# Kernel optimization log

Hardware: AMD Instinct MI355X
Metric: run time of the kernel (lower is better)

The kernel has to match this reference:

```python
import jax, jax.numpy as jnp
import numpy as np

B, T = 4, 1024
H, C, DK, DV = 12, 4096, 64, 64
DIM = H * DK  # 768


def setup_inputs() -> dict:
    key = jax.random.key(0)
    k1, k2, k3 = jax.random.split(key, 3)
    x = jax.random.normal(k1, (B, T, DIM), dtype=jnp.float32)
    # key_embed initialized with kaiming_uniform in torch; uniform in [-bound, bound]
    bound = float(np.sqrt(3.0) * np.sqrt(2.0) / np.sqrt(C * DK))
    key_embed = jax.random.uniform(k2, (H, C, DK), minval=-bound, maxval=bound, dtype=jnp.float32)
    values = jax.random.normal(k3, (H, C, DV), dtype=jnp.float32)
    mask = jnp.ones((B, T), dtype=jnp.int32)
    return {"x": x, "mask": mask, "key_embed": key_embed, "values": values, "key_optim": 0}


def reference(x, mask, key_embed, values, key_optim):
    # x: [b, t, h*dk]; key_embed: [h, c, dk]; values: [h, c, dv]
    b, t, _ = x.shape
    h, c, dk = key_embed.shape
    dv = values.shape[-1]
    x = x.astype(jnp.float32)
    # 'b t (h d) -> h (b t) d'
    xh = x.reshape(b, t, h, dk).transpose(2, 0, 1, 3).reshape(h, b * t, dk)
    # squared-L2 nearest codebook entry (argmax of -cdist == argmin of squared dist)
    x2 = jnp.sum(xh * xh, axis=-1, keepdims=True)          # [h, n, 1]
    e2 = jnp.sum(key_embed * key_embed, axis=-1)           # [h, c]
    dots = jnp.einsum('hnd,hcd->hnc', xh, key_embed)       # [h, n, c]
    d2 = x2 - 2.0 * dots + e2[:, None, :]                  # [h, n, c]
    ind = jnp.argmin(d2, axis=-1)                          # [h, n]
    # gather per-head learned values: values[h, ind[h, n], :]
    memories = jnp.take_along_axis(values, ind[..., None], axis=1)  # [h, n, dv]
    # 'h (b t) dv -> b t (h dv)'  (decoder == 'mlp')
    memories = memories.transpose(1, 0, 2).reshape(b, t, h * dv)
    return memories
```

## Files before the change

### kernel.cpp

```cpp
#include <hip/hip_runtime.h>


#define HEADS 12
#define CODES 4096
#define DKI   64
#define DVI   64
#define DIMX  768
#define TAUS  3.84e-3f
#define WLCAP 32768
#define NPARTS 16

typedef _Float16 f16x8 __attribute__((ext_vector_type(8)));
typedef float f32x4 __attribute__((ext_vector_type(4)));

__device__ __forceinline__ unsigned short f2bf(float f) {
    unsigned int u = __float_as_uint(f);
    return (unsigned short)((u + 0x7fff + ((u >> 16) & 1)) >> 16);
}
__device__ __forceinline__ unsigned short f2h(float f) {
    _Float16 h = (_Float16)f;
    unsigned short u;
    __builtin_memcpy(&u, &h, 2);
    return u;
}
__device__ __forceinline__ f16x8 as_f16x8(uint4 v) {
    union { uint4 u; f16x8 h; } c; c.u = v; return c.h;
}

__device__ __forceinline__ float np_sumsq64(const float* __restrict__ a) {
#pragma clang fp contract(off)
    float r[8];
#pragma unroll
    for (int j = 0; j < 8; ++j) r[j] = a[j] * a[j];
#pragma unroll
    for (int i = 8; i < 64; i += 8)
#pragma unroll
        for (int j = 0; j < 8; ++j) r[j] += a[i + j] * a[i + j];
    return ((r[0] + r[1]) + (r[2] + r[3])) + ((r[4] + r[5]) + (r[6] + r[7]));
}

__device__ __forceinline__ float np_dot64(const float* __restrict__ xx,
                                          const float* __restrict__ ee) {
#pragma clang fp contract(off)
    float S0 = 0.f, S1 = 0.f, S2 = 0.f, S3 = 0.f;
#pragma unroll
    for (int t = 0; t < 64; t += 16) {
        float p[16];
#pragma unroll
        for (int j = 0; j < 16; ++j) p[j] = xx[t + j] * ee[t + j];
        S0 = p[0] + (p[4] + (p[8]  + (p[12] + S0)));
        S1 = p[1] + (p[5] + (p[9]  + (p[13] + S1)));
        S2 = p[2] + (p[6] + (p[10] + (p[14] + S2)));
        S3 = p[3] + (p[7] + (p[11] + (p[15] + S3)));
    }
    return (S0 + S1) + (S2 + S3);
}

__global__ __launch_bounds__(256) void prep_ke(const float* __restrict__ ke,
                                               uint4* __restrict__ EhT,
                                               float* __restrict__ e2np,
                                               unsigned short* __restrict__ m2bf,
                                               int* __restrict__ wl_count) {
    __shared__ float sq[32][64];
    __shared__ float rr[32][8];
    const int t = threadIdx.x;
    if (blockIdx.x == 0 && t < 2) wl_count[t] = 0;
    const int p = t >> 5, cw = t & 31;
    const int idx = blockIdx.x * 32 + cw;

    float er[8];
    {
        const float4* p4 = reinterpret_cast<const float4*>(
            ke + (size_t)idx * DKI + p * 8);
        float4 v0 = p4[0], v1 = p4[1];
        er[0] = v0.x; er[1] = v0.y; er[2] = v0.z; er[3] = v0.w;
        er[4] = v1.x; er[5] = v1.y; er[6] = v1.z; er[7] = v1.w;
    }
    {
#pragma clang fp contract(off)
#pragma unroll
        for (int j = 0; j < 8; ++j) sq[cw][p * 8 + j] = er[j] * er[j];
    }
    __syncthreads();
    {
#pragma clang fp contract(off)
        float r = sq[cw][p];
#pragma unroll
        for (int k = 1; k < 8; ++k) r = r + sq[cw][k * 8 + p];
        rr[cw][p] = r;
    }
    __syncthreads();
    const int h = idx >> 12, c = idx & 4095;
    const int half = c >> 11, gg = (c & 2047) >> 5;
    const int pair = h * 2 + half;
    if (p == 0) {
#pragma clang fp contract(off)
        float e2 = ((rr[cw][0] + rr[cw][1]) + (rr[cw][2] + rr[cw][3])) +
                   ((rr[cw][4] + rr[cw][5]) + (rr[cw][6] + rr[cw][7]));
        e2np[idx] = e2;
        m2bf[(size_t)pair * 2048 + (c & 2047)] = f2bf(-32.f * e2);
    }

    unsigned int hb[8];
#pragma unroll
    for (int j = 0; j < 8; ++j)
        hb[j] = f2h(er[j] * 64.f);
    uint4 hv;
    hv.x = hb[0] | (hb[1] << 16); hv.y = hb[2] | (hb[3] << 16);
    hv.z = hb[4] | (hb[5] << 16); hv.w = hb[6] | (hb[7] << 16);
    EhT[((size_t)(pair * 64 + gg) * 8 + p) * 32 + cw] = hv;
}

#define MERGE3(v1o, i1o, v2o, i2o, v3o,                                   \
               a1, j1, a2, j2, a3, b1, k1, b2, k2, b3)                    \
    {                                                                     \
        bool t1 = (b1) > (a1);                                            \
        float _l1 = t1 ? (a1) : (b1);  int _k1 = t1 ? (j1) : (k1);        \
        (v1o) = t1 ? (b1) : (a1);      (i1o) = t1 ? (k1) : (j1);          \
        float _s2 = t1 ? (b2) : (a2);  int _u2 = t1 ? (k2) : (j2);        \
        bool t2 = _s2 > _l1;                                              \
        (v2o) = t2 ? _s2 : _l1;        (i2o) = t2 ? _u2 : _k1;            \
        float _l2 = t2 ? _l1 : _s2;                                       \
        float _s3 = t2 ? (t1 ? (b3) : (a3)) : (t1 ? (a2) : (b2));         \
        bool t3 = _s3 > _l2;                                              \
        (v3o) = t3 ? _s3 : _l2;                                           \
    }

__global__ __launch_bounds__(256, 4) void dkvb_pass1(
        const float* __restrict__ x,
        const char* __restrict__ EhT,
        const unsigned short* __restrict__ m2bf,
        const float* __restrict__ values,
        int* __restrict__ wl_count,
        int* __restrict__ wl,
        int* __restrict__ wlc,
        int* __restrict__ wlf,
        unsigned long long* __restrict__ res,
        int* __restrict__ pcnt,
        float* __restrict__ out) {
    __shared__ float sb1[4][32], sb2[4][32], sb3[4][32];
    __shared__ int   sbi[4][32];
    __shared__ int   fin[32];

    const int tid  = threadIdx.x;
    const int h    = blockIdx.x % 12;
    const int qb   = blockIdx.x / 12;
    const int w    = tid >> 6;
    const int lane = tid & 63;
    const int cl16 = lane & 15;
    const int kg   = lane >> 4;
    const int q0   = qb * 32;
    const int pair = h * 2 + (w >> 1);
    const int qoff = (w >> 1) * 2048 + (w & 1) * 1024;

    f16x8 ah[2][2];
#pragma unroll
    for (int T = 0; T < 2; ++T) {
        const float* xrow = x + (size_t)(q0 + T * 16 + cl16) * DIMX + h * DKI;
#pragma unroll
        for (int t = 0; t < 2; ++t) {
            const float* p = xrow + t * 32 + kg * 8;
            float4 v0 = *reinterpret_cast<const float4*>(p);
            float4 v1 = *reinterpret_cast<const float4*>(p + 4);
            f16x8 hv;
            hv[0] = (_Float16)v0.x; hv[1] = (_Float16)v0.y;
            hv[2] = (_Float16)v0.z; hv[3] = (_Float16)v0.w;
            hv[4] = (_Float16)v1.x; hv[5] = (_Float16)v1.y;
            hv[6] = (_Float16)v1.z; hv[7] = (_Float16)v1.w;
            ah[T][t] = hv;
        }
    }

    const char* gE = EhT + (size_t)(pair * 64 + (w & 1) * 32) * 4096
                   + (size_t)kg * 512 + (size_t)cl16 * 16;
    const unsigned short* gm = m2bf + (size_t)pair * 2048
                             + (size_t)(w & 1) * 1024 + cl16;

    float bv[2][4], bv2[2][4], bv3[2][4];
#pragma unroll
    for (int T = 0; T < 2; ++T)
#pragma unroll
        for (int r = 0; r < 4; ++r) {
            bv[T][r] = -1e30f; bv2[T][r] = -1e30f; bv3[T][r] = -1e30f;
        }

    auto LOADF = [&](int i, uint4& b0, uint4& b1, unsigned short& mA) {
        const char* p = gE + (size_t)(i >> 1) * 4096 + (size_t)(i & 1) * 256;
        b0 = *reinterpret_cast<const uint4*>(p);
        b1 = *reinterpret_cast<const uint4*>(p + 2048);
        mA = gm[i * 16];
    };
    auto COMPUTE = [&](int i, uint4 b0, uint4 b1, unsigned short mA) {
        float m2f = __uint_as_float((unsigned)mA << 16);
        f32x4 macc;
        macc[0] = m2f; macc[1] = m2f; macc[2] = m2f; macc[3] = m2f;
        unsigned enc = (unsigned)i;
#pragma unroll
        for (int T = 0; T < 2; ++T) {
            f32x4 acc;
            acc = __builtin_amdgcn_mfma_f32_16x16x32_f16(ah[T][0], as_f16x8(b0),
                                                         macc, 0, 0, 0);
            acc = __builtin_amdgcn_mfma_f32_16x16x32_f16(ah[T][1], as_f16x8(b1),
                                                         acc, 0, 0, 0);
#pragma unroll
            for (int r = 0; r < 4; ++r) {
                float sp = __uint_as_float(
                    (__float_as_uint(acc[r]) & 0xFFFFFFC0u) | enc);
                bv3[T][r] = __builtin_amdgcn_fmed3f(bv3[T][r], sp, bv2[T][r]);
                bv2[T][r] = __builtin_amdgcn_fmed3f(bv2[T][r], sp, bv[T][r]);
                bv[T][r]  = fmaxf(bv[T][r], sp);
            }
        }
    };

    uint4 A0, A1, B0, B1, C0, C1, D0, D1;
    unsigned short Am, Bm, Cm, Dm;
    LOADF(0, A0, A1, Am);
    LOADF(1, B0, B1, Bm);
    LOADF(2, C0, C1, Cm);
#pragma unroll 1
    for (int i = 0; i < 56; i += 4) {
        LOADF(i + 3, D0, D1, Dm);
        COMPUTE(i, A0, A1, Am);
        LOADF(i + 4, A0, A1, Am);
        COMPUTE(i + 1, B0, B1, Bm);
        LOADF(i + 5, B0, B1, Bm);
        COMPUTE(i + 2, C0, C1, Cm);
        LOADF(i + 6, C0, C1, Cm);
        COMPUTE(i + 3, D0, D1, Dm);
    }
    LOADF(59, D0, D1, Dm);
    COMPUTE(56, A0, A1, Am);
    LOADF(60, A0, A1, Am);
    COMPUTE(57, B0, B1, Bm);
    LOADF(61, B0, B1, Bm);
    COMPUTE(58, C0, C1, Cm);
    LOADF(62, C0, C1, Cm);
    COMPUTE(59, D0, D1, Dm);
    LOADF(63, D0, D1, Dm);
    COMPUTE(60, A0, A1, Am);
    COMPUTE(61, B0, B1, Bm);
    COMPUTE(62, C0, C1, Cm);
    COMPUTE(63, D0, D1, Dm);

    int bi1[2][4], bi2[2][4];
#pragma unroll
    for (int T = 0; T < 2; ++T)
#pragma unroll
        for (int r = 0; r < 4; ++r) {
            bi1[T][r] = (int)(__float_as_uint(bv[T][r])  & 63u) * 16 + cl16 + qoff;
            bi2[T][r] = (int)(__float_as_uint(bv2[T][r]) & 63u) * 16 + cl16 + qoff;
        }
#pragma unroll
    for (int T = 0; T < 2; ++T)
#pragma unroll
        for (int r = 0; r < 4; ++r) {
#pragma unroll
            for (int m = 1; m <= 8; m <<= 1) {
                float p1 = __shfl_xor(bv[T][r],  m, 64);
                float p2 = __shfl_xor(bv2[T][r], m, 64);
                float p3 = __shfl_xor(bv3[T][r], m, 64);
                int   q1 = __shfl_xor(bi1[T][r], m, 64);
                int   q2 = __shfl_xor(bi2[T][r], m, 64);
                bool t1 = (p1 > bv[T][r]) || (p1 == bv[T][r] && q1 < bi1[T][r]);
                float w1 = t1 ? p1 : bv[T][r];   int j1 = t1 ? q1 : bi1[T][r];
                float l1 = t1 ? bv[T][r] : p1;   int k1 = t1 ? bi1[T][r] : q1;
                float s2 = t1 ? p2 : bv2[T][r];  int u2 = t1 ? q2 : bi2[T][r];
                bool t2 = s2 > l1;
                float w2 = t2 ? s2 : l1;         int j2 = t2 ? u2 : k1;
                float l2 = t2 ? l1 : s2;
                float s3 = t2 ? (t1 ? p3 : bv3[T][r]) : (t1 ? bv2[T][r] : p2);
                bool t3 = s3 > l2;
                float w3 = t3 ? s3 : l2;
                bv[T][r] = w1; bi1[T][r] = j1;
                bv2[T][r] = w2; bi2[T][r] = j2;
                bv3[T][r] = w3;
            }
        }
    if (cl16 == 0) {
#pragma unroll
        for (int T = 0; T < 2; ++T)
#pragma unroll
            for (int r = 0; r < 4; ++r) {
                int row = T * 16 + kg * 4 + r;
                sb1[w][row] = bv[T][r];
                sb2[w][row] = bv2[T][r];
                sb3[w][row] = bv3[T][r];
                sbi[w][row] = (bi1[T][r] << 16) | bi2[T][r];
            }
    }
    __syncthreads();

    if (tid < 32) {
        float v1[4], v2[4], v3[4]; int i1[4], i2[4];
#pragma unroll
        for (int qd = 0; qd < 4; ++qd) {
            v1[qd] = sb1[qd][tid]; v2[qd] = sb2[qd][tid]; v3[qd] = sb3[qd][tid];
            int pk = sbi[qd][tid];
            i1[qd] = (pk >> 16) & 0xffff; i2[qd] = pk & 0xffff;
        }
        float m1a, m2a, m3a, m1b, m2b, m3b, V1, V2, V3;
        int j1a, j2a, j1b, j2b, I1, I2;
        MERGE3(m1a, j1a, m2a, j2a, m3a,
               v1[0], i1[0], v2[0], i2[0], v3[0],
               v1[1], i1[1], v2[1], i2[1], v3[1]);
        MERGE3(m1b, j1b, m2b, j2b, m3b,
               v1[2], i1[2], v2[2], i2[2], v3[2],
               v1[3], i1[3], v2[3], i2[3], v3[3]);
        MERGE3(V1, I1, V2, I2, V3,
               m1a, j1a, m2a, j2a, m3a,
               m1b, j1b, m2b, j2b, m3b);
        fin[tid] = I1;
        if (V1 - V2 < TAUS) {
            if (V1 - V3 < TAUS) {
                int slot = atomicAdd(wl_count + 1, 1);
                if (slot < WLCAP) {
                    wlf[slot]  = (h << 16) | (q0 + tid);
                    res[slot]  = ~0ULL;
                    pcnt[slot] = 0;
                }
            } else {
                int slot = atomicAdd(wl_count, 1);
                if (slot < WLCAP) {
                    wl[slot]  = (h << 16) | (q0 + tid);
                    wlc[slot] = (I1 << 16) | I2;
                }
            }
        }
    }
    __syncthreads();

#pragma unroll
    for (int k = 0; k < 2; ++k) {
        int f   = tid + k * 256;
        int row = f >> 4;
        int cl  = (f & 15) << 2;
        int idx = fin[row];
        float4 v = *reinterpret_cast<const float4*>(
            values + (size_t)h * CODES * DVI + (size_t)idx * DVI + cl);
        *reinterpret_cast<float4*>(
            out + (size_t)(q0 + row) * DIMX + h * DVI + cl) = v;
    }
}

__global__ __launch_bounds__(256) void post_check(const float* __restrict__ x,
                                                  const float* __restrict__ ke,
                                                  const float* __restrict__ e2np,
                                                  const float* __restrict__ values,
                                                  const int* __restrict__ wl_count,
                                                  const int* __restrict__ wl,
                                                  const int* __restrict__ wlc,
                                                  const int* __restrict__ wlf,
                                                  unsigned long long* __restrict__ res,
                                                  int* __restrict__ pcnt,
                                                  float* __restrict__ out) {
    __shared__ float xs[4][DKI];
    const int t = threadIdx.x, w = t >> 6, lane = t & 63;
    int cnt0 = wl_count[0]; if (cnt0 > WLCAP) cnt0 = WLCAP;
    int cnt1 = wl_count[1]; if (cnt1 > WLCAP) cnt1 = WLCAP;
    const int total = cnt0 + cnt1 * NPARTS;

    for (int item = blockIdx.x * 4 + w; item < total; item += gridDim.x * 4) {
        if (item < cnt0) {
            int ent = wl[item];
            int h = ent >> 16, nq = ent & 0xffff;
            int cp = wlc[item];
            if (lane < 16) {
                float4 v = *reinterpret_cast<const float4*>(
                    x + (size_t)nq * DIMX + h * DKI + lane * 4);
                *reinterpret_cast<float4*>(&xs[w][lane * 4]) = v;
            }
            asm volatile("s_waitcnt lgkmcnt(0)" ::: "memory");
            __builtin_amdgcn_sched_barrier(0);

            int i1 = (cp >> 16) & 0xffff, i2 = cp & 0xffff;
            float d2 = 0.f;
            if (lane < 2) {
                int myc = lane ? i2 : i1;
                float er[DKI];
                const float4* p = reinterpret_cast<const float4*>(
                    ke + ((size_t)h * CODES + myc) * DKI);
#pragma unroll
                for (int i = 0; i < DKI / 4; ++i) {
                    float4 v = p[i];
                    er[i * 4 + 0] = v.x; er[i * 4 + 1] = v.y;
                    er[i * 4 + 2] = v.z; er[i * 4 + 3] = v.w;
                }
                float x2 = np_sumsq64(xs[w]);
                float dot = np_dot64(xs[w], er);
                {
#pragma clang fp contract(off)
                    d2 = (x2 - 2.0f * dot) + e2np[h * CODES + myc];
                }
            }
            float dA = __shfl(d2, 0, 64);
            float dB = __shfl(d2, 1, 64);
            int win = (dB < dA || (dB == dA && i2 < i1)) ? i2 : i1;
            if (lane < 16) {
                float4 v = *reinterpret_cast<const float4*>(
                    values + ((size_t)h * CODES + win) * DVI + lane * 4);
                *reinterpret_cast<float4*>(
                    out + (size_t)nq * DIMX + h * DVI + lane * 4) = v;
            }
        } else {
            const int j = item - cnt0;
            const int e = j >> 4, part = j & (NPARTS - 1);
            const int ent = wlf[e];
            const int h = ent >> 16, nq = ent & 0xffff;
            if (lane < 16) {
                float4 v = *reinterpret_cast<const float4*>(
                    x + (size_t)nq * DIMX + h * DKI + lane * 4);
                *reinterpret_cast<float4*>(&xs[w][lane * 4]) = v;
            }
            asm volatile("s_waitcnt lgkmcnt(0)" ::: "memory");
            __builtin_amdgcn_sched_barrier(0);

            float x2 = np_sumsq64(xs[w]);
            unsigned long long best = ~0ULL;
#pragma unroll 1
            for (int it = 0; it < 4; ++it) {
                int c = part * 256 + it * 64 + lane;
                float er[DKI];
                const float4* p = reinterpret_cast<const float4*>(
                    ke + ((size_t)h * CODES + c) * DKI);
#pragma unroll
                for (int i = 0; i < DKI / 4; ++i) {
                    float4 v = p[i];
                    er[i * 4 + 0] = v.x; er[i * 4 + 1] = v.y;
                    er[i * 4 + 2] = v.z; er[i * 4 + 3] = v.w;
                }
                float dot = np_dot64(xs[w], er);
                float d2;
                {
#pragma clang fp contract(off)
                    d2 = (x2 - 2.0f * dot) + e2np[h * CODES + c];
                }
                unsigned u = __float_as_uint(d2);
                unsigned key = (u & 0x80000000u) ? ~u : (u | 0x80000000u);
                unsigned long long pk =
                    ((unsigned long long)key << 32) | (unsigned)c;
                best = pk < best ? pk : best;
            }
#pragma unroll
            for (int m = 1; m <= 32; m <<= 1) {
                unsigned long long o =
                    (unsigned long long)__shfl_xor((long long)best, m, 64);
                best = o < best ? o : best;
            }
            int lastflag = 0;
            if (lane == 0) {
                atomicMin(res + e, best);
                __threadfence();
                lastflag = (atomicAdd(pcnt + e, 1) == NPARTS - 1);
            }
            lastflag = __shfl(lastflag, 0, 64);
            if (lastflag) {
                unsigned long long fin = 0;
                if (lane == 0) {
                    __threadfence();
                    fin = atomicMin(res + e, ~0ULL);
                }
                int win = (int)(__shfl((long long)fin, 0, 64) & 0xFFFFFFFFLL);
                if (lane < 16) {
                    float4 v = *reinterpret_cast<const float4*>(
                        values + ((size_t)h * CODES + win) * DVI + lane * 4);
                    *reinterpret_cast<float4*>(
                        out + (size_t)nq * DIMX + h * DVI + lane * 4) = v;
                }
            }
        }
    }
}

extern "C" void kernel_launch(void* const* d_in, const int* in_sizes, int n_in,
                              void* d_out, int out_size, void* d_ws, size_t ws_size,
                              hipStream_t stream) {
    const float* x      = (const float*)d_in[0];
    const float* ke     = (const float*)d_in[2];
    const float* values = (const float*)d_in[3];
    float* out = (float*)d_out;

    char* ws = (char*)d_ws;
    float* e2np          = (float*)ws;          ws += (size_t)HEADS * CODES * 4;
    unsigned short* m2bf = (unsigned short*)ws; ws += (size_t)HEADS * 2 * 2048 * 2;
    int*   wl_count      = (int*)ws;            ws += 64;
    int*   wl            = (int*)ws;            ws += (size_t)WLCAP * 4;
    int*   wlc           = (int*)ws;            ws += (size_t)WLCAP * 4;
    int*   wlf           = (int*)ws;            ws += (size_t)WLCAP * 4;
    unsigned long long* res = (unsigned long long*)ws; ws += (size_t)WLCAP * 8;
    int*   pcnt          = (int*)ws;            ws += (size_t)WLCAP * 4;
    char*  EhT           = ws;                  ws += (size_t)HEADS * CODES * 128;

    prep_ke<<<dim3(HEADS * CODES / 32), dim3(256), 0, stream>>>(
        ke, (uint4*)EhT, e2np, m2bf, wl_count);
    dkvb_pass1<<<dim3(1536), dim3(256), 0, stream>>>(
        x, EhT, m2bf, values, wl_count, wl, wlc, wlf, res, pcnt, out);
    post_check<<<dim3(2048), dim3(256), 0, stream>>>(
        x, ke, e2np, values, wl_count, wl, wlc, wlf, res, pcnt, out);
}
```

Measured before the change: 168.0 us.

## Double query tile per block in pass1 and batch 32 rechecks per wave

Result: slower. 184.9 us (+10.1%).

```diff
diff --git a/kernel.cpp b/kernel.cpp
--- a/kernel.cpp
+++ b/kernel.cpp
@@ -126,7 +126,7 @@
         (v3o) = t3 ? _s3 : _l2;                                           \
     }
 
-__global__ __launch_bounds__(256, 4) void dkvb_pass1(
+__global__ __launch_bounds__(256, 3) void dkvb_pass1(
         const float* __restrict__ x,
         const char* __restrict__ EhT,
         const unsigned short* __restrict__ m2bf,
@@ -138,9 +138,9 @@
         unsigned long long* __restrict__ res,
         int* __restrict__ pcnt,
         float* __restrict__ out) {
-    __shared__ float sb1[4][32], sb2[4][32], sb3[4][32];
-    __shared__ int   sbi[4][32];
-    __shared__ int   fin[32];
+    __shared__ float sb1[4][64], sb2[4][64], sb3[4][64];
+    __shared__ int   sbi[4][64];
+    __shared__ int   fin[64];
 
     const int tid  = threadIdx.x;
     const int h    = blockIdx.x % 12;
@@ -149,13 +149,13 @@
     const int lane = tid & 63;
     const int cl16 = lane & 15;
     const int kg   = lane >> 4;
-    const int q0   = qb * 32;
+    const int q0   = qb * 64;
     const int pair = h * 2 + (w >> 1);
     const int qoff = (w >> 1) * 2048 + (w & 1) * 1024;
 
-    f16x8 ah[2][2];
-#pragma unroll
-    for (int T = 0; T < 2; ++T) {
+    f16x8 ah[4][2];
+#pragma unroll
+    for (int T = 0; T < 4; ++T) {
         const float* xrow = x + (size_t)(q0 + T * 16 + cl16) * DIMX + h * DKI;
 #pragma unroll
         for (int t = 0; t < 2; ++t) {
@@ -176,9 +176,9 @@
     const unsigned short* gm = m2bf + (size_t)pair * 2048
                              + (size_t)(w & 1) * 1024 + cl16;
 
-    float bv[2][4], bv2[2][4], bv3[2][4];
-#pragma unroll
-    for (int T = 0; T < 2; ++T)
+    float bv[4][4], bv2[4][4], bv3[4][4];
+#pragma unroll
+    for (int T = 0; T < 4; ++T)
 #pragma unroll
         for (int r = 0; r < 4; ++r) {
             bv[T][r] = -1e30f; bv2[T][r] = -1e30f; bv3[T][r] = -1e30f;
@@ -196,7 +196,7 @@
         macc[0] = m2f; macc[1] = m2f; macc[2] = m2f; macc[3] = m2f;
         unsigned enc = (unsigned)i;
 #pragma unroll
-        for (int T = 0; T < 2; ++T) {
+        for (int T = 0; T < 4; ++T) {
             f32x4 acc;
             acc = __builtin_amdgcn_mfma_f32_16x16x32_f16(ah[T][0], as_f16x8(b0),
                                                          macc, 0, 0, 0);
@@ -243,16 +243,16 @@
     COMPUTE(62, C0, C1, Cm);
     COMPUTE(63, D0, D1, Dm);
 
-    int bi1[2][4], bi2[2][4];
-#pragma unroll
-    for (int T = 0; T < 2; ++T)
+    int bi1[4][4], bi2[4][4];
+#pragma unroll
+    for (int T = 0; T < 4; ++T)
 #pragma unroll
         for (int r = 0; r < 4; ++r) {
             bi1[T][r] = (int)(__float_as_uint(bv[T][r])  & 63u) * 16 + cl16 + qoff;
             bi2[T][r] = (int)(__float_as_uint(bv2[T][r]) & 63u) * 16 + cl16 + qoff;
         }
 #pragma unroll
-    for (int T = 0; T < 2; ++T)
+    for (int T = 0; T < 4; ++T)
 #pragma unroll
         for (int r = 0; r < 4; ++r) {
 #pragma unroll
@@ -279,7 +279,7 @@
         }
     if (cl16 == 0) {
 #pragma unroll
-        for (int T = 0; T < 2; ++T)
+        for (int T = 0; T < 4; ++T)
 #pragma unroll
             for (int r = 0; r < 4; ++r) {
                 int row = T * 16 + kg * 4 + r;
@@ -291,7 +291,7 @@
     }
     __syncthreads();
 
-    if (tid < 32) {
+    if (tid < 64) {
         float v1[4], v2[4], v3[4]; int i1[4], i2[4];
 #pragma unroll
         for (int qd = 0; qd < 4; ++qd) {
@@ -331,7 +331,7 @@
     __syncthreads();
 
 #pragma unroll
-    for (int k = 0; k < 2; ++k) {
+    for (int k = 0; k < 4; ++k) {
         int f   = tid + k * 256;
         int row = f >> 4;
         int cl  = (f & 15) << 2;
@@ -355,55 +355,75 @@
                                                   int* __restrict__ pcnt,
                                                   float* __restrict__ out) {
     __shared__ float xs[4][DKI];
+    __shared__ int   ewin[4][32];
+    __shared__ int   einfo[4][32];
     const int t = threadIdx.x, w = t >> 6, lane = t & 63;
     int cnt0 = wl_count[0]; if (cnt0 > WLCAP) cnt0 = WLCAP;
     int cnt1 = wl_count[1]; if (cnt1 > WLCAP) cnt1 = WLCAP;
-    const int total = cnt0 + cnt1 * NPARTS;
+    const int D = (cnt0 + 31) >> 5;
+    const int total = D + cnt1 * NPARTS;
 
     for (int item = blockIdx.x * 4 + w; item < total; item += gridDim.x * 4) {
-        if (item < cnt0) {
-            int ent = wl[item];
+        if (item < D) {
+            const int base = item << 5;
+            const int e = base + (lane >> 1);
+            const bool act = e < cnt0;
+            int ent = act ? wl[e] : 0;
+            int cp  = act ? wlc[e] : 0;
             int h = ent >> 16, nq = ent & 0xffff;
-            int cp = wlc[item];
-            if (lane < 16) {
-                float4 v = *reinterpret_cast<const float4*>(
-                    x + (size_t)nq * DIMX + h * DKI + lane * 4);
-                *reinterpret_cast<float4*>(&xs[w][lane * 4]) = v;
+            int myc = (lane & 1) ? (cp & 0xffff) : ((cp >> 16) & 0xffff);
+            float d2 = 3.4e38f;
+            if (act) {
+                float xr[DKI], er[DKI];
+                const float4* px = reinterpret_cast<const float4*>(
+                    x + (size_t)nq * DIMX + h * DKI);
+                const float4* pe = reinterpret_cast<const float4*>(
+                    ke + ((size_t)h * CODES + myc) * DKI);
+#pragma unroll
+                for (int i = 0; i < DKI / 4; ++i) {
+                    float4 a = px[i], b = pe[i];
+                    xr[i * 4 + 0] = a.x; xr[i * 4 + 1] = a.y;
+                    xr[i * 4 + 2] = a.z; xr[i * 4 + 3] = a.w;
+                    er[i * 4 + 0] = b.x; er[i * 4 + 1] = b.y;
+                    er[i * 4 + 2] = b.z; er[i * 4 + 3] = b.w;
+                }
+                float x2 = np_sumsq64(xr);
+                float dot = np_dot64(xr, er);
+                {
+#pragma clang fp contract(off)
+                    d2 = (x2 - 2.0f * dot) + e2np[h * CODES + myc];
+                }
+            }
+            float dO = __shfl_xor(d2, 1, 64);
+            int   cO = __shfl_xor(myc, 1, 64);
+            int i1 = (lane & 1) ? cO : myc;
+            int i2 = (lane & 1) ? myc : cO;
+            float dA = (lane & 1) ? dO : d2;
+            float dB = (lane & 1) ? d2 : dO;
+            int win = (dB < dA || (dB == dA && i2 < i1)) ? i2 : i1;
+            if ((lane & 1) == 0) {
+                ewin [w][lane >> 1] = win;
+                einfo[w][lane >> 1] = ent;
             }
             asm volatile("s_waitcnt lgkmcnt(0)" ::: "memory");
             __builtin_amdgcn_sched_barrier(0);
-
-            int i1 = (cp >> 16) & 0xffff, i2 = cp & 0xffff;
-            float d2 = 0.f;
-            if (lane < 2) {
-                int myc = lane ? i2 : i1;
-                float er[DKI];
-                const float4* p = reinterpret_cast<const float4*>(
-                    ke + ((size_t)h * CODES + myc) * DKI);
-#pragma unroll
-                for (int i = 0; i < DKI / 4; ++i) {
-                    float4 v = p[i];
-                    er[i * 4 + 0] = v.x; er[i * 4 + 1] = v.y;
-                    er[i * 4 + 2] = v.z; er[i * 4 + 3] = v.w;
-                }
-                float x2 = np_sumsq64(xs[w]);
-                float dot = np_dot64(xs[w], er);
-                {
-#pragma clang fp contract(off)
-                    d2 = (x2 - 2.0f * dot) + e2np[h * CODES + myc];
-                }
-            }
-            float dA = __shfl(d2, 0, 64);
-            float dB = __shfl(d2, 1, 64);
-            int win = (dB < dA || (dB == dA && i2 < i1)) ? i2 : i1;
-            if (lane < 16) {
-                float4 v = *reinterpret_cast<const float4*>(
-                    values + ((size_t)h * CODES + win) * DVI + lane * 4);
-                *reinterpret_cast<float4*>(
-                    out + (size_t)nq * DIMX + h * DVI + lane * 4) = v;
+#pragma unroll
+            for (int j2 = 0; j2 < 8; ++j2) {
+                int fidx = j2 * 64 + lane;
+                int el = fidx >> 4;
+                int cl = (fidx & 15) << 2;
+                if (base + el < cnt0) {
+                    int info = einfo[w][el];
+                    int hh = info >> 16, qq = info & 0xffff;
+                    int cc = ewin[w][el];
+                    float4 v = *reinterpret_cast<const float4*>(
+                        values + ((size_t)hh * CODES + cc) * DVI + cl);
+                    *reinterpret_cast<float4*>(
+                        out + (size_t)qq * DIMX + hh * DVI + cl) = v;
+                }
             }
         } else {
-            const int j = item - cnt0;
+            const int j = item - D;
             const int e = j >> 4, part = j & (NPARTS - 1);
             const int ent = wlf[e];
             const int h = ent >> 16, nq = ent & 0xffff;
@@ -493,7 +513,7 @@
 
     prep_ke<<<dim3(HEADS * CODES / 32), dim3(256), 0, stream>>>(
         ke, (uint4*)EhT, e2np, m2bf, wl_count);
-    dkvb_pass1<<<dim3(1536), dim3(256), 0, stream>>>(
+    dkvb_pass1<<<dim3(768), dim3(256), 0, stream>>>(
         x, EhT, m2bf, values, wl_count, wl, wlc, wlf, res, pcnt, out);
     post_check<<<dim3(2048), dim3(256), 0, stream>>>(
         x, ke, e2np, values, wl_count, wl, wlc, wlf, res, pcnt, out);
```
